# Kernel optimization log

Hardware: AMD Instinct MI355X
Metric: run time of the kernel (lower is better)

## Reference

```python
import jax, jax.numpy as jnp
import numpy as np


def _sage_mean_layer(x, src, dst, W_self, W_neigh, b):
    # DGL SAGEConv('mean'): h_neigh = mean_{u in N(v)} x_u ; out = x@W_self + h_neigh@W_neigh + b
    n = x.shape[0]
    msg_sum = jax.ops.segment_sum(x[src], dst, num_segments=n)          # [N, D] scatter-add
    deg = jax.ops.segment_sum(jnp.ones_like(dst, dtype=x.dtype), dst, num_segments=n)
    h_neigh = msg_sum / jnp.maximum(deg, 1.0)[:, None]                   # zero-degree nodes -> 0
    return x @ W_self + h_neigh @ W_neigh + b


def setup_inputs() -> dict:
    key = jax.random.key(0)
    ks = jax.random.split(key, 9)
    N, E, D_in, D_hid, D_out = 50000, 800000, 128, 128, 128
    s = lambda d: 1.0 / np.sqrt(d)
    return {
        "x": jax.random.normal(ks[0], (N, D_in), dtype=jnp.float32),
        "src": jax.random.randint(ks[1], (E,), 0, N, dtype=jnp.int32),
        "dst": jax.random.randint(ks[2], (E,), 0, N, dtype=jnp.int32),
        "W1_self": jax.random.uniform(ks[3], (D_in, D_hid), jnp.float32, -s(D_in), s(D_in)),
        "W1_neigh": jax.random.uniform(ks[4], (D_in, D_hid), jnp.float32, -s(D_in), s(D_in)),
        "b1": jnp.zeros((D_hid,), jnp.float32),
        "W2_self": jax.random.uniform(ks[5], (D_hid, D_out), jnp.float32, -s(D_hid), s(D_hid)),
        "W2_neigh": jax.random.uniform(ks[6], (D_hid, D_out), jnp.float32, -s(D_hid), s(D_hid)),
        "b2": jnp.zeros((D_out,), jnp.float32),
    }


def reference(x, src, dst, W1_self, W1_neigh, b1, W2_self, W2_neigh, b2):
    # layer 1: SAGEConv -> ELU (dropout is identity in eval mode)
    h = jax.nn.elu(_sage_mean_layer(x, src, dst, W1_self, W1_neigh, b1))
    # layer 2: is_out_layer=True -> no activation
    return _sage_mean_layer(h, src, dst, W2_self, W2_neigh, b2)
```

## Files before the change

### kernel.cpp

```cpp
#include <hip/hip_runtime.h>
#include <hip/hip_bf16.h>
#include <math.h>

#define DD 128
#define CAP 64

typedef __attribute__((ext_vector_type(8))) short short8;
typedef __attribute__((ext_vector_type(4))) float floatx4;
typedef __attribute__((ext_vector_type(8))) unsigned short ushortx8;

__global__ __launch_bounds__(256) void prologue_kernel(
        const int* __restrict__ src, const int* __restrict__ dst,
        int* __restrict__ cnt, ushort* __restrict__ slot16, int E,
        const float* __restrict__ x, ushort* __restrict__ Xc, int n,
        const float* __restrict__ W1a, const float* __restrict__ W1b,
        const float* __restrict__ W2a, const float* __restrict__ W2b,
        ushort* __restrict__ Wp1, ushort* __restrict__ Wp2,
        int fb, int cb) {
    int b = blockIdx.x;
    if (b < fb) {
        int base = (b * 256 + threadIdx.x) * 4;
        if (base + 3 < E) {
            int4 d4 = *(const int4*)&dst[base];
            int4 s4 = *(const int4*)&src[base];
            int p0 = atomicAdd(&cnt[d4.x], 1);
            int p1 = atomicAdd(&cnt[d4.y], 1);
            int p2 = atomicAdd(&cnt[d4.z], 1);
            int p3 = atomicAdd(&cnt[d4.w], 1);
            if (p0 < CAP) slot16[(size_t)d4.x * CAP + p0] = (ushort)s4.x;
            if (p1 < CAP) slot16[(size_t)d4.y * CAP + p1] = (ushort)s4.y;
            if (p2 < CAP) slot16[(size_t)d4.z * CAP + p2] = (ushort)s4.z;
            if (p3 < CAP) slot16[(size_t)d4.w * CAP + p3] = (ushort)s4.w;
        } else {
            for (int e = base; e < E; ++e) {
                int d = dst[e];
                int p = atomicAdd(&cnt[d], 1);
                if (p < CAP) slot16[(size_t)d * CAP + p] = (ushort)src[e];
            }
        }
        return;
    }
    if (b < fb + cb) {
        int i = (b - fb) * 256 + threadIdx.x;
        if (i >= n * 32) return;
        int node = i >> 5;
        int col = (i & 31) * 4;
        float4 v = *(const float4*)&x[(size_t)node * DD + col];
        __hip_bfloat16 b0 = __float2bfloat16(v.x), b1 = __float2bfloat16(v.y);
        __hip_bfloat16 b2 = __float2bfloat16(v.z), b3 = __float2bfloat16(v.w);
        ushort4 o;
        o.x = *(ushort*)&b0; o.y = *(ushort*)&b1; o.z = *(ushort*)&b2; o.w = *(ushort*)&b3;
        size_t ns = (size_t)n * 32;
        *(ushort4*)&Xc[(size_t)(col >> 5) * ns + (size_t)node * 32 + (col & 31)] = o;
        return;
    }
    int gid = (b - fb - cb) * 256 + threadIdx.x;
    int layer = gid >> 15;
    int r = gid & 32767;
    int j = r & 7;
    int lane = (r >> 3) & 63;
    int nt = (r >> 9) & 7;
    int ks = r >> 12;
    int k = ks * 32 + (lane >> 4) * 8 + j;
    int col = nt * 16 + (lane & 15);
    const float* W = layer ? (k < 128 ? W2a : W2b) : (k < 128 ? W1a : W1b);
    float v = W[(k & 127) * DD + col];
    __hip_bfloat16 bb = __float2bfloat16(v);
    (layer ? Wp2 : Wp1)[r] = *(ushort*)&bb;
}

#define BF2F(u) __uint_as_float((unsigned)(u) << 16)

__global__ __launch_bounds__(256) void agg_mean_kernel(
        const ushort* __restrict__ Xc, const int* __restrict__ cnt,
        const ushort* __restrict__ slot16, ushort* __restrict__ Hnc, int n) {
    int pass = blockIdx.x & 3;
    int lane = threadIdx.x & 63;
    int g = lane >> 2;
    int q = lane & 3;
    int v = (blockIdx.x >> 2) * 64 + (threadIdx.x >> 6) * 16 + g;
    if (v >= n) return;
    size_t ns = (size_t)n * 32;
    const ushort* Xp = Xc + (size_t)pass * ns;
    int d = cnt[v];
    if (d > CAP) d = CAP;

    float acc[8];
#pragma unroll
    for (int j = 0; j < 8; ++j) acc[j] = 0.f;

    const ushort* srow = slot16 + (size_t)v * CAP;
    int i = 0;
    for (; i + 2 <= d; i += 2) {
        int u0 = (int)srow[i];
        int u1 = (int)srow[i + 1];
        ushortx8 y0 = *(const ushortx8*)&Xp[(size_t)u0 * 32 + q * 8];
        ushortx8 y1 = *(const ushortx8*)&Xp[(size_t)u1 * 32 + q * 8];
#pragma unroll
        for (int j = 0; j < 8; ++j)
            acc[j] += BF2F((ushort)y0[j]) + BF2F((ushort)y1[j]);
    }
    if (i < d) {
        int u = (int)srow[i];
        ushortx8 y = *(const ushortx8*)&Xp[(size_t)u * 32 + q * 8];
#pragma unroll
        for (int j = 0; j < 8; ++j) acc[j] += BF2F((ushort)y[j]);
    }

    float inv = 1.0f / (float)(d > 0 ? d : 1);
    ushort tmp[8];
#pragma unroll
    for (int j = 0; j < 8; ++j) {
        __hip_bfloat16 b = __float2bfloat16(acc[j] * inv);
        tmp[j] = *(ushort*)&b;
    }
    uint4 ov;
    ov.x = (unsigned)tmp[0] | ((unsigned)tmp[1] << 16);
    ov.y = (unsigned)tmp[2] | ((unsigned)tmp[3] << 16);
    ov.z = (unsigned)tmp[4] | ((unsigned)tmp[5] << 16);
    ov.w = (unsigned)tmp[6] | ((unsigned)tmp[7] << 16);
    *(uint4*)&Hnc[(size_t)pass * ns + (size_t)v * 32 + q * 8] = ov;
}

__global__ __launch_bounds__(256) void gemm_fused_kernel(
        const ushort* __restrict__ Xc, const ushort* __restrict__ Hnc,
        const ushort* __restrict__ Wp, const float* __restrict__ bias,
        ushort* __restrict__ out_bf16c, float* __restrict__ out_f32,
        int n, int nstrips, int do_elu) {
    int strip = blockIdx.x * 4 + (threadIdx.x >> 6);
    if (strip >= nstrips) return;
    int lane = threadIdx.x & 63;
    int m = lane & 15;
    int quad = lane >> 4;
    size_t ns = (size_t)n * 32;
    const size_t row0 = (size_t)strip * 16;

    floatx4 acc[8];
#pragma unroll
    for (int t = 0; t < 8; ++t) acc[t] = (floatx4){0.f, 0.f, 0.f, 0.f};

#pragma unroll
    for (int ks = 0; ks < 8; ++ks) {
        const ushort* ap = (ks < 4 ? Xc + (size_t)ks * ns : Hnc + (size_t)(ks - 4) * ns)
                           + (row0 + m) * 32 + quad * 8;
        short8 a = *(const short8*)ap;
        const ushort* wp = Wp + ((size_t)(ks * 8) * 64 + lane) * 8;
#pragma unroll
        for (int nt = 0; nt < 8; ++nt) {
            short8 b = *(const short8*)(wp + (size_t)nt * 64 * 8);
            acc[nt] = __builtin_amdgcn_mfma_f32_16x16x32_bf16(a, b, acc[nt], 0, 0, 0);
        }
    }

#pragma unroll
    for (int nt = 0; nt < 8; ++nt) {
        int col = nt * 16 + m;
        float bv = bias[col];
#pragma unroll
        for (int r = 0; r < 4; ++r) {
            size_t row = row0 + quad * 4 + r;
            float v = acc[nt][r] + bv;
            if (do_elu) v = v > 0.f ? v : expm1f(v);
            if (out_f32) {
                out_f32[row * DD + col] = v;
            } else {
                __hip_bfloat16 b = __float2bfloat16(v);
                out_bf16c[(size_t)(nt >> 1) * ns + row * 32 + (nt & 1) * 16 + m] = *(ushort*)&b;
            }
        }
    }
}


extern "C" void kernel_launch(void* const* d_in, const int* in_sizes, int n_in,
                              void* d_out, int out_size, void* d_ws, size_t ws_size,
                              hipStream_t stream) {
    const float* x   = (const float*)d_in[0];
    const int*   src = (const int*)d_in[1];
    const int*   dst = (const int*)d_in[2];
    const float* W1s = (const float*)d_in[3];
    const float* W1n = (const float*)d_in[4];
    const float* b1  = (const float*)d_in[5];
    const float* W2s = (const float*)d_in[6];
    const float* W2n = (const float*)d_in[7];
    const float* b2  = (const float*)d_in[8];
    float* out = (float*)d_out;

    const int N = in_sizes[0] / DD;
    const int E = in_sizes[1];

    char* ws = (char*)d_ws;
    int*    cnt    = (int*)ws;    ws += (size_t)N * 4;
    ushort* slot16 = (ushort*)ws; ws += (size_t)N * CAP * 2;
    ushort* Wp1    = (ushort*)ws; ws += 65536;
    ushort* Wp2    = (ushort*)ws; ws += 65536;
    ushort* Xc     = (ushort*)ws; ws += (size_t)N * DD * 2;
    ushort* Hnc    = (ushort*)ws; ws += (size_t)N * DD * 2;
    ushort* H1c    = (ushort*)ws; ws += (size_t)N * DD * 2;

    (void)hipMemsetAsync(cnt, 0, (size_t)N * 4, stream);
    const int fb = (E / 4 + 255) / 256;
    const int cb = (N * 32 + 255) / 256;
    const int pb = 256;
    prologue_kernel<<<fb + cb + pb, 256, 0, stream>>>(
        src, dst, cnt, slot16, E, x, Xc, N, W1s, W1n, W2s, W2n, Wp1, Wp2, fb, cb);

    const int nstrips = N / 16;
    const int gb = (nstrips + 3) / 4;
    const int ab = 4 * ((N + 63) / 64);

    agg_mean_kernel<<<ab, 256, 0, stream>>>(Xc, cnt, slot16, Hnc, N);
    gemm_fused_kernel<<<gb, 256, 0, stream>>>(Xc, Hnc, Wp1, b1, H1c, nullptr, N, nstrips, 1);

    agg_mean_kernel<<<ab, 256, 0, stream>>>(H1c, cnt, slot16, Hnc, N);
    gemm_fused_kernel<<<gb, 256, 0, stream>>>(H1c, Hnc, Wp2, b2, nullptr, out, N, nstrips, 0);
}
```

Before: 246.0 us.

## Bucket edges by destination shard before building adjacency slots

Edge-to-slot construction becomes two passes. The first buckets (dst,src) pairs into 8 destination shards, using LDS counters and one global cursor per shard per block. The second pass runs the per-destination atomics and slot writes shard by shard, so each group of blocks touches a narrower address range that may stay cache-resident. The cnt memset is folded into the first kernel, at the cost of an extra kernel launch and an extra write/read of an 8*E pair buffer.

```diff
diff --git a/kernel.cpp b/kernel.cpp
--- a/kernel.cpp
+++ b/kernel.cpp
@@ -4,44 +4,72 @@
 
 #define DD 128
 #define CAP 64
+#define NSHARD 8
 
 typedef __attribute__((ext_vector_type(8))) short short8;
 typedef __attribute__((ext_vector_type(4))) float floatx4;
 typedef __attribute__((ext_vector_type(8))) unsigned short ushortx8;
 
-__global__ __launch_bounds__(256) void prologue_kernel(
+__global__ __launch_bounds__(256) void p1_kernel(
         const int* __restrict__ src, const int* __restrict__ dst,
-        int* __restrict__ cnt, ushort* __restrict__ slot16, int E,
+        unsigned int* __restrict__ pairs, int* __restrict__ cursor,
+        int* __restrict__ cnt, int E,
         const float* __restrict__ x, ushort* __restrict__ Xc, int n,
         const float* __restrict__ W1a, const float* __restrict__ W1b,
         const float* __restrict__ W2a, const float* __restrict__ W2b,
         ushort* __restrict__ Wp1, ushort* __restrict__ Wp2,
-        int fb, int cb) {
+        int bb, int zb, int cb, int shard_size) {
     int b = blockIdx.x;
-    if (b < fb) {
+    if (b < bb) {
+        __shared__ int lcnt[NSHARD], lbase[NSHARD], lofs[NSHARD];
+        if (threadIdx.x < NSHARD) { lcnt[threadIdx.x] = 0; lofs[threadIdx.x] = 0; }
+        __syncthreads();
         int base = (b * 256 + threadIdx.x) * 4;
+        int ds[4], ss[4], sh[4];
         if (base + 3 < E) {
             int4 d4 = *(const int4*)&dst[base];
             int4 s4 = *(const int4*)&src[base];
-            int p0 = atomicAdd(&cnt[d4.x], 1);
-            int p1 = atomicAdd(&cnt[d4.y], 1);
-            int p2 = atomicAdd(&cnt[d4.z], 1);
-            int p3 = atomicAdd(&cnt[d4.w], 1);
-            if (p0 < CAP) slot16[(size_t)d4.x * CAP + p0] = (ushort)s4.x;
-            if (p1 < CAP) slot16[(size_t)d4.y * CAP + p1] = (ushort)s4.y;
-            if (p2 < CAP) slot16[(size_t)d4.z * CAP + p2] = (ushort)s4.z;
-            if (p3 < CAP) slot16[(size_t)d4.w * CAP + p3] = (ushort)s4.w;
+            ds[0] = d4.x; ds[1] = d4.y; ds[2] = d4.z; ds[3] = d4.w;
+            ss[0] = s4.x; ss[1] = s4.y; ss[2] = s4.z; ss[3] = s4.w;
         } else {
-            for (int e = base; e < E; ++e) {
-                int d = dst[e];
-                int p = atomicAdd(&cnt[d], 1);
-                if (p < CAP) slot16[(size_t)d * CAP + p] = (ushort)src[e];
+#pragma unroll
+            for (int j = 0; j < 4; ++j) {
+                int e = base + j;
+                ds[j] = (e < E) ? dst[e] : -1;
+                ss[j] = (e < E) ? src[e] : 0;
+            }
+        }
+#pragma unroll
+        for (int j = 0; j < 4; ++j) {
+            sh[j] = (ds[j] >= 0) ? (ds[j] / shard_size) : -1;
+            if (sh[j] >= 0) atomicAdd(&lcnt[sh[j]], 1);
+        }
+        __syncthreads();
+        if (threadIdx.x < NSHARD) lbase[threadIdx.x] = atomicAdd(&cursor[threadIdx.x], lcnt[threadIdx.x]);
+        __syncthreads();
+#pragma unroll
+        for (int j = 0; j < 4; ++j) {
+            if (sh[j] >= 0) {
+                int pos = lbase[sh[j]] + atomicAdd(&lofs[sh[j]], 1);
+                unsigned int dloc = (unsigned int)(ds[j] - sh[j] * shard_size);
+                pairs[(size_t)sh[j] * E + pos] = (dloc << 16) | (unsigned int)ss[j];
             }
         }
         return;
     }
-    if (b < fb + cb) {
-        int i = (b - fb) * 256 + threadIdx.x;
+    b -= bb;
+    if (b < zb) {
+        int i = (b * 256 + threadIdx.x) * 4;
+        if (i + 3 < n) {
+            *(int4*)&cnt[i] = make_int4(0, 0, 0, 0);
+        } else {
+            for (int j = i; j < n; ++j) cnt[j] = 0;
+        }
+        return;
+    }
+    b -= zb;
+    if (b < cb) {
+        int i = b * 256 + threadIdx.x;
         if (i >= n * 32) return;
         int node = i >> 5;
         int col = (i & 31) * 4;
@@ -54,7 +82,8 @@
         *(ushort4*)&Xc[(size_t)(col >> 5) * ns + (size_t)node * 32 + (col & 31)] = o;
         return;
     }
-    int gid = (b - fb - cb) * 256 + threadIdx.x;
+    b -= cb;
+    int gid = b * 256 + threadIdx.x;
     int layer = gid >> 15;
     int r = gid & 32767;
     int j = r & 7;
@@ -65,8 +94,46 @@
     int col = nt * 16 + (lane & 15);
     const float* W = layer ? (k < 128 ? W2a : W2b) : (k < 128 ? W1a : W1b);
     float v = W[(k & 127) * DD + col];
-    __hip_bfloat16 bb = __float2bfloat16(v);
-    (layer ? Wp2 : Wp1)[r] = *(ushort*)&bb;
+    __hip_bfloat16 bb16 = __float2bfloat16(v);
+    (layer ? Wp2 : Wp1)[r] = *(ushort*)&bb16;
+}
+
+__global__ __launch_bounds__(256) void p2_fill_kernel(
+        const unsigned int* __restrict__ pairs, const int* __restrict__ cursor,
+        int* __restrict__ cnt, ushort* __restrict__ slot16,
+        int E, int shard_size, int nchunk) {
+    int s = blockIdx.x & (NSHARD - 1);
+    int chunk = blockIdx.x >> 3;
+    int m = cursor[s];
+    int lo = s * shard_size;
+    const unsigned int* P = pairs + (size_t)s * E;
+    int per = (((m + nchunk - 1) / nchunk) + 3) & ~3;
+    int beg = chunk * per;
+    int end = beg + per; if (end > m) end = m;
+    for (int i = beg + threadIdx.x * 4; i < end; i += 1024) {
+        if (i + 3 < end) {
+            uint4 p4 = *(const uint4*)&P[i];
+            int d0 = lo + (int)(p4.x >> 16);
+            int d1 = lo + (int)(p4.y >> 16);
+            int d2 = lo + (int)(p4.z >> 16);
+            int d3 = lo + (int)(p4.w >> 16);
+            int q0 = atomicAdd(&cnt[d0], 1);
+            int q1 = atomicAdd(&cnt[d1], 1);
+            int q2 = atomicAdd(&cnt[d2], 1);
+            int q3 = atomicAdd(&cnt[d3], 1);
+            if (q0 < CAP) slot16[(size_t)d0 * CAP + q0] = (ushort)(p4.x & 0xffff);
+            if (q1 < CAP) slot16[(size_t)d1 * CAP + q1] = (ushort)(p4.y & 0xffff);
+            if (q2 < CAP) slot16[(size_t)d2 * CAP + q2] = (ushort)(p4.z & 0xffff);
+            if (q3 < CAP) slot16[(size_t)d3 * CAP + q3] = (ushort)(p4.w & 0xffff);
+        } else {
+            for (int j = i; j < end; ++j) {
+                unsigned int p = P[j];
+                int d = lo + (int)(p >> 16);
+                int q = atomicAdd(&cnt[d], 1);
+                if (q < CAP) slot16[(size_t)d * CAP + q] = (ushort)(p & 0xffff);
+            }
+        }
+    }
 }
 
 #define BF2F(u) __uint_as_float((unsigned)(u) << 16)
@@ -192,18 +259,28 @@
     char* ws = (char*)d_ws;
     int*    cnt    = (int*)ws;    ws += (size_t)N * 4;
     ushort* slot16 = (ushort*)ws; ws += (size_t)N * CAP * 2;
+    int*    cursor = (int*)ws;    ws += 64;
+    unsigned int* pairs = (unsigned int*)ws; ws += (size_t)NSHARD * E * 4;
     ushort* Wp1    = (ushort*)ws; ws += 65536;
     ushort* Wp2    = (ushort*)ws; ws += 65536;
     ushort* Xc     = (ushort*)ws; ws += (size_t)N * DD * 2;
     ushort* Hnc    = (ushort*)ws; ws += (size_t)N * DD * 2;
     ushort* H1c    = (ushort*)ws; ws += (size_t)N * DD * 2;
 
-    (void)hipMemsetAsync(cnt, 0, (size_t)N * 4, stream);
-    const int fb = (E / 4 + 255) / 256;
+    const int shard_size = (N + NSHARD - 1) / NSHARD;
+    (void)hipMemsetAsync(cursor, 0, NSHARD * 4, stream);
+
+    const int bb = (E + 1023) / 1024;
+    const int zb = (N + 1023) / 1024;
     const int cb = (N * 32 + 255) / 256;
     const int pb = 256;
-    prologue_kernel<<<fb + cb + pb, 256, 0, stream>>>(
-        src, dst, cnt, slot16, E, x, Xc, N, W1s, W1n, W2s, W2n, Wp1, Wp2, fb, cb);
+    p1_kernel<<<bb + zb + cb + pb, 256, 0, stream>>>(
+        src, dst, pairs, cursor, cnt, E, x, Xc, N,
+        W1s, W1n, W2s, W2n, Wp1, Wp2, bb, zb, cb, shard_size);
+
+    const int nchunk = 64;
+    p2_fill_kernel<<<nchunk * NSHARD, 256, 0, stream>>>(
+        pairs, cursor, cnt, slot16, E, shard_size, nchunk);
 
     const int nstrips = N / 16;
     const int gb = (nstrips + 3) / 4;
```

Result: slower. 251.7 us (+2.3%).

## Assign aggregation feature-chunk passes per XCC via persistent work-stealing blocks

Applied to the files above, without the earlier changes.

The aggregation kernel becomes a persistent kernel of 2048 blocks. Each block reads its XCC id and starts on the feature chunk (pass) matching that id, so gathers from one 3.2MB chunk tend to stay within one XCD's L2. Blocks pull 64-node work units from a per-pass global atomic counter and move on to the other passes once theirs is exhausted. This aims to raise L2 hit rate on the random neighbor gathers, at the cost of atomic traffic and two block barriers per work unit. It also depends on the hardware XCC-id register.

```diff
diff --git a/kernel.cpp b/kernel.cpp
--- a/kernel.cpp
+++ b/kernel.cpp
@@ -73,53 +73,67 @@
 
 __global__ __launch_bounds__(256) void agg_mean_kernel(
         const ushort* __restrict__ Xc, const int* __restrict__ cnt,
-        const ushort* __restrict__ slot16, ushort* __restrict__ Hnc, int n) {
-    int pass = blockIdx.x & 3;
+        const ushort* __restrict__ slot16, ushort* __restrict__ Hnc,
+        int* __restrict__ q, int n, int NB) {
+    __shared__ int s_u;
+    int xcc = 0;
+    asm volatile("s_getreg_b32 %0, hwreg(HW_REG_XCC_ID)" : "=s"(xcc));
     int lane = threadIdx.x & 63;
     int g = lane >> 2;
-    int q = lane & 3;
-    int v = (blockIdx.x >> 2) * 64 + (threadIdx.x >> 6) * 16 + g;
-    if (v >= n) return;
+    int sq = lane & 3;
+    int wave = threadIdx.x >> 6;
     size_t ns = (size_t)n * 32;
-    const ushort* Xp = Xc + (size_t)pass * ns;
-    int d = cnt[v];
-    if (d > CAP) d = CAP;
-
-    float acc[8];
-#pragma unroll
-    for (int j = 0; j < 8; ++j) acc[j] = 0.f;
-
-    const ushort* srow = slot16 + (size_t)v * CAP;
-    int i = 0;
-    for (; i + 2 <= d; i += 2) {
-        int u0 = (int)srow[i];
-        int u1 = (int)srow[i + 1];
-        ushortx8 y0 = *(const ushortx8*)&Xp[(size_t)u0 * 32 + q * 8];
-        ushortx8 y1 = *(const ushortx8*)&Xp[(size_t)u1 * 32 + q * 8];
-#pragma unroll
-        for (int j = 0; j < 8; ++j)
-            acc[j] += BF2F((ushort)y0[j]) + BF2F((ushort)y1[j]);
-    }
-    if (i < d) {
-        int u = (int)srow[i];
-        ushortx8 y = *(const ushortx8*)&Xp[(size_t)u * 32 + q * 8];
-#pragma unroll
-        for (int j = 0; j < 8; ++j) acc[j] += BF2F((ushort)y[j]);
-    }
-
-    float inv = 1.0f / (float)(d > 0 ? d : 1);
-    ushort tmp[8];
-#pragma unroll
-    for (int j = 0; j < 8; ++j) {
-        __hip_bfloat16 b = __float2bfloat16(acc[j] * inv);
-        tmp[j] = *(ushort*)&b;
-    }
-    uint4 ov;
-    ov.x = (unsigned)tmp[0] | ((unsigned)tmp[1] << 16);
-    ov.y = (unsigned)tmp[2] | ((unsigned)tmp[3] << 16);
-    ov.z = (unsigned)tmp[4] | ((unsigned)tmp[5] << 16);
-    ov.w = (unsigned)tmp[6] | ((unsigned)tmp[7] << 16);
-    *(uint4*)&Hnc[(size_t)pass * ns + (size_t)v * 32 + q * 8] = ov;
+
+    for (int t = 0; t < 4; ++t) {
+        int pass = (xcc + t) & 3;
+        const ushort* Xp = Xc + (size_t)pass * ns;
+        ushort* Hp = Hnc + (size_t)pass * ns;
+        for (;;) {
+            __syncthreads();
+            if (threadIdx.x == 0) s_u = atomicAdd(&q[pass], 1);
+            __syncthreads();
+            int u = s_u;
+            if (u >= NB) break;
+            int v = u * 64 + wave * 16 + g;
+            if (v < n) {
+                int d = cnt[v];
+                if (d > CAP) d = CAP;
+                float acc[8];
+#pragma unroll
+                for (int j = 0; j < 8; ++j) acc[j] = 0.f;
+                const ushort* srow = slot16 + (size_t)v * CAP;
+                int i = 0;
+                for (; i + 2 <= d; i += 2) {
+                    int u0 = (int)srow[i];
+                    int u1 = (int)srow[i + 1];
+                    ushortx8 y0 = *(const ushortx8*)&Xp[(size_t)u0 * 32 + sq * 8];
+                    ushortx8 y1 = *(const ushortx8*)&Xp[(size_t)u1 * 32 + sq * 8];
+#pragma unroll
+                    for (int j = 0; j < 8; ++j)
+                        acc[j] += BF2F((ushort)y0[j]) + BF2F((ushort)y1[j]);
+                }
+                if (i < d) {
+                    int u0 = (int)srow[i];
+                    ushortx8 y = *(const ushortx8*)&Xp[(size_t)u0 * 32 + sq * 8];
+#pragma unroll
+                    for (int j = 0; j < 8; ++j) acc[j] += BF2F((ushort)y[j]);
+                }
+                float inv = 1.0f / (float)(d > 0 ? d : 1);
+                ushort tmp[8];
+#pragma unroll
+                for (int j = 0; j < 8; ++j) {
+                    __hip_bfloat16 b = __float2bfloat16(acc[j] * inv);
+                    tmp[j] = *(ushort*)&b;
+                }
+                uint4 ov;
+                ov.x = (unsigned)tmp[0] | ((unsigned)tmp[1] << 16);
+                ov.y = (unsigned)tmp[2] | ((unsigned)tmp[3] << 16);
+                ov.z = (unsigned)tmp[4] | ((unsigned)tmp[5] << 16);
+                ov.w = (unsigned)tmp[6] | ((unsigned)tmp[7] << 16);
+                *(uint4*)&Hp[(size_t)v * 32 + sq * 8] = ov;
+            }
+        }
+    }
 }
 
 __global__ __launch_bounds__(256) void gemm_fused_kernel(
@@ -192,6 +206,7 @@
     char* ws = (char*)d_ws;
     int*    cnt    = (int*)ws;    ws += (size_t)N * 4;
     ushort* slot16 = (ushort*)ws; ws += (size_t)N * CAP * 2;
+    int*    q      = (int*)ws;    ws += 64;
     ushort* Wp1    = (ushort*)ws; ws += 65536;
     ushort* Wp2    = (ushort*)ws; ws += 65536;
     ushort* Xc     = (ushort*)ws; ws += (size_t)N * DD * 2;
@@ -199,6 +214,7 @@
     ushort* H1c    = (ushort*)ws; ws += (size_t)N * DD * 2;
 
     (void)hipMemsetAsync(cnt, 0, (size_t)N * 4, stream);
+    (void)hipMemsetAsync(q, 0, 64, stream);
     const int fb = (E / 4 + 255) / 256;
     const int cb = (N * 32 + 255) / 256;
     const int pb = 256;
@@ -207,11 +223,12 @@
 
     const int nstrips = N / 16;
     const int gb = (nstrips + 3) / 4;
-    const int ab = 4 * ((N + 63) / 64);
-
-    agg_mean_kernel<<<ab, 256, 0, stream>>>(Xc, cnt, slot16, Hnc, N);
+    const int NB = (N + 63) / 64;
+    const int ab = 2048;
+
+    agg_mean_kernel<<<ab, 256, 0, stream>>>(Xc, cnt, slot16, Hnc, q, N, NB);
     gemm_fused_kernel<<<gb, 256, 0, stream>>>(Xc, Hnc, Wp1, b1, H1c, nullptr, N, nstrips, 1);
 
-    agg_mean_kernel<<<ab, 256, 0, stream>>>(H1c, cnt, slot16, Hnc, N);
+    agg_mean_kernel<<<ab, 256, 0, stream>>>(H1c, cnt, slot16, Hnc, q + 4, N, NB);
     gemm_fused_kernel<<<gb, 256, 0, stream>>>(H1c, Hnc, Wp2, b2, nullptr, out, N, nstrips, 0);
 }
```

Result: slower. 476.9 us (+93.9%).
